# Kernel optimization log

Measured on AMD Instinct MI355X. Metric: run time of the kernel, lower is better.

## Reference

```python
import jax, jax.numpy as jnp
import numpy as np

# Performer/FAVOR+ style linear attention constants (from module __init__)
A_CONST = 0.1
S_CONST = 1.0
B_CONST = (S_CONST * (1.0 - 4.0 * A_CONST)) ** 0.5  # sqrt(0.6)
C_CONST = -(S_CONST + 1.0) / 2.0                    # -1.0

R = 256     # number of random features
D = 64      # head / feature dim
L = 65536   # sequence length
DV = 64     # value dim
SCALE = 0.125  # keep ||q||^2 ~ 1 so exp stays well-conditioned


def setup_inputs() -> dict:
    key = jax.random.key(0)
    kq, kk, kv, kw = jax.random.split(key, 4)
    Q = jax.random.normal(kq, (D, L), dtype=jnp.float32) * SCALE
    K = jax.random.normal(kk, (D, L), dtype=jnp.float32) * SCALE
    V = jax.random.normal(kv, (L, DV), dtype=jnp.float32)
    W = jax.random.normal(kw, (R, D), dtype=jnp.float32)  # random feature projections
    return {"Q": Q, "K": K, "V": V, "W": W}


def _phi(W, X, c):
    # X: [d, L]; W: [r, d] -> features [r, L]
    d = X.shape[0]
    D_norm = (1.0 - 4.0 * A_CONST) ** (d / 4.0)  # pow(pow(1-4A,0.25), d)
    sq = jnp.sum(X * X, axis=0)                  # [L], diag of X^T X
    return D_norm * jnp.exp(A_CONST + B_CONST * (W @ X) + c * sq)


def reference(Q, K, V, W):
    phiK = _phi(W, K, C_CONST * S_CONST)  # f2: [r, Lk]
    kv = phiK @ V                          # [r, dv]
    phiQ = _phi(W, Q, C_CONST)             # f1: [r, Lq]
    return phiQ.T @ kv                     # [Lq, dv]
```

## Files before the change

### kernel.cpp

```cpp
#include <hip/hip_runtime.h>

typedef _Float16 f16;
typedef __attribute__((ext_vector_type(8))) _Float16 f16x8;
typedef __attribute__((ext_vector_type(4))) _Float16 f16x4;
typedef __attribute__((ext_vector_type(4))) float f32x4;

#define BARRIER()                                              \
    do {                                                       \
        asm volatile("s_waitcnt lgkmcnt(0)" ::: "memory");     \
        __builtin_amdgcn_s_barrier();                          \
        __builtin_amdgcn_sched_barrier(0);                     \
    } while (0)

namespace {
constexpr int kL   = 65536;
constexpr int kR   = 256;
constexpr int kD   = 64;
constexpr int kDV  = 64;

constexpr int kABlocks = 512;
constexpr int kBBlocks = 512;
constexpr int kRBlocks = 128;

constexpr float kBc   = 0.7745966692414834f;
constexpr float kBase0 = -1.1417405264f;
constexpr float kOutScale = 9.5367431640625e-7f;
}

__global__ __launch_bounds__(512, 2)
void favor_kv(const float* __restrict__ Kg, const float* __restrict__ Vg,
              const float* __restrict__ Wg, f16* __restrict__ partials)
{
    __shared__ f16 sXt[2][64 * 64];
    __shared__ f16 sVt[2][64 * 64];
    __shared__ f16 sPhi[256 * 64];
    __shared__ float sRed[2][8 * 64];
    __shared__ float sRedT[2][64];

    const int tid  = threadIdx.x;
    const int w    = tid >> 6;
    const int lane = tid & 63;
    const int l15  = lane & 15;
    const int lhi  = lane >> 4;
    const int blk  = blockIdx.x;
    const int lblk = blk * 128;

    const int scol  = lane;
    const int dbase = w * 8;
    const int wr = w >> 1;
    const int wc = w & 1;

    float ka[2][8], va[2][8];
#pragma unroll
    for (int c = 0; c < 2; ++c) {
        const int l0 = lblk + c * 64;
#pragma unroll
        for (int j = 0; j < 8; ++j) ka[c][j] = Kg[(dbase + j) * kL + l0 + scol];
#pragma unroll
        for (int j = 0; j < 8; ++j) va[c][j] = Vg[(size_t)(l0 + dbase + j) * kDV + scol];
    }

    f16x8 wfrag[2][2];
#pragma unroll
    for (int ri = 0; ri < 2; ++ri)
#pragma unroll
        for (int ks = 0; ks < 2; ++ks) {
            const float* p = Wg + (32 * w + 16 * ri + l15) * kD + 32 * ks + 8 * lhi;
            f16x8 v;
#pragma unroll
            for (int j = 0; j < 8; ++j) v[j] = (f16)p[j];
            wfrag[ri][ks] = v;
        }

    f32x4 acc[4][2];
#pragma unroll
    for (int a = 0; a < 4; ++a)
#pragma unroll
        for (int d = 0; d < 2; ++d) { f32x4 z0 = {0.f, 0.f, 0.f, 0.f}; acc[a][d] = z0; }

    auto stage = [&](int c) {
        float s = 0.f;
        f16x8 hk, hv;
#pragma unroll
        for (int j = 0; j < 8; ++j) {
            const float x = ka[c][j];
            s += x * x;
            hk[j] = (f16)x;
            hv[j] = (f16)va[c][j];
        }
        sRed[c][w * 64 + scol] = s;
        *(f16x8*)&sXt[c][scol * 64 + (dbase ^ ((scol & 7) << 3))] = hk;
        *(f16x8*)&sVt[c][scol * 64 + (dbase ^ ((scol & 7) << 3))] = hv;
    };

    auto norms = [&](int c) {
        float sqv = 0.f;
#pragma unroll
        for (int g = 0; g < 8; ++g) sqv += sRed[c][g * 64 + lane];
        sRedT[c][lane] = sqv;
    };

    auto zphi = [&](int c) {
        f16x8 bfr[2][4];
#pragma unroll
        for (int ks = 0; ks < 2; ++ks)
#pragma unroll
            for (int lf = 0; lf < 4; ++lf) {
                const int row = 16 * lf + l15;
                bfr[ks][lf] = *(const f16x8*)&sXt[c][row * 64 + ((32 * ks + 8 * lhi) ^ ((row & 7) << 3))];
            }
#pragma unroll
        for (int ri = 0; ri < 2; ++ri) {
            f32x4 z[4];
#pragma unroll
            for (int lf = 0; lf < 4; ++lf) { f32x4 z0 = {0.f, 0.f, 0.f, 0.f}; z[lf] = z0; }
            __builtin_amdgcn_s_setprio(1);
#pragma unroll
            for (int ks = 0; ks < 2; ++ks)
#pragma unroll
                for (int lf = 0; lf < 4; ++lf)
                    z[lf] = __builtin_amdgcn_mfma_f32_16x16x32_f16(bfr[ks][lf], wfrag[ri][ks], z[lf], 0, 0, 0);
            __builtin_amdgcn_s_setprio(0);
            const int r = 32 * w + 16 * ri + l15;
#pragma unroll
            for (int lf = 0; lf < 4; ++lf) {
                const f32x4 sq4 = *(const f32x4*)&sRedT[c][16 * lf + 4 * lhi];
                f16x4 ph;
#pragma unroll
                for (int j = 0; j < 4; ++j)
                    ph[j] = (f16)__expf(fmaf(z[lf][j], kBc, kBase0 - sq4[j]));
                const int lbase = 16 * lf + 4 * lhi;
                *(f16x4*)&sPhi[r * 64 + (lbase ^ ((r & 7) << 3))] = ph;
            }
        }
    };

    auto pv = [&](int c) {
        __builtin_amdgcn_s_setprio(1);
#pragma unroll
        for (int ks = 0; ks < 2; ++ks) {
            f16x8 af[4], bf[2];
#pragma unroll
            for (int ai = 0; ai < 4; ++ai) {
                const int r = 64 * wr + 16 * ai + l15;
                af[ai] = *(const f16x8*)&sPhi[r * 64 + ((32 * ks + 8 * lhi) ^ ((r & 7) << 3))];
            }
#pragma unroll
            for (int di = 0; di < 2; ++di) {
                const int dv = 32 * wc + 16 * di + l15;
                bf[di] = *(const f16x8*)&sVt[c][dv * 64 + ((32 * ks + 8 * lhi) ^ ((dv & 7) << 3))];
            }
#pragma unroll
            for (int ai = 0; ai < 4; ++ai)
#pragma unroll
                for (int di = 0; di < 2; ++di)
                    acc[ai][di] = __builtin_amdgcn_mfma_f32_16x16x32_f16(af[ai], bf[di], acc[ai][di], 0, 0, 0);
        }
        __builtin_amdgcn_s_setprio(0);
    };

    stage(0);
    BARRIER();
    norms(0);
    zphi(0);
    stage(1);
    BARRIER();
    norms(1);
    pv(0);
    BARRIER();
    zphi(1);
    BARRIER();
    pv(1);

    f16* po = partials + (size_t)blk * (kR * kDV);
#pragma unroll
    for (int ai = 0; ai < 4; ++ai)
#pragma unroll
        for (int di = 0; di < 2; ++di) {
            const int dv = 32 * wc + 16 * di + l15;
            f16x4 pk;
#pragma unroll
            for (int j = 0; j < 4; ++j) pk[j] = (f16)acc[ai][di][j];
            *(f16x4*)&po[dv * kR + 64 * wr + 16 * ai + 4 * lhi] = pk;
        }
}

__global__ __launch_bounds__(512)
void favor_reduce(const f16* __restrict__ partials, f16* __restrict__ kvT,
                  const float* __restrict__ Wg, f16* __restrict__ Wp)
{
    __shared__ float sAcc[32][128];
    const int tid  = threadIdx.x;
    const int slot = tid & 15;
    const int g    = tid >> 4;

    if (blockIdx.x == 0) {
#pragma unroll
        for (int it = 0; it < 4; ++it) {
            const int idx    = tid + it * 512;
            const int fragid = idx >> 6;
            const int ln     = idx & 63;
            const int rf = fragid >> 1, ks = fragid & 1;
            const float* src = Wg + (16 * rf + (ln & 15)) * kD + 32 * ks + 8 * (ln >> 4);
            f16x8 v;
#pragma unroll
            for (int j = 0; j < 8; ++j) v[j] = (f16)src[j];
            *(f16x8*)&Wp[(size_t)idx * 8] = v;
        }
    }

    const size_t obase = (size_t)blockIdx.x * 128 + slot * 8;
    float a[8] = {0.f, 0.f, 0.f, 0.f, 0.f, 0.f, 0.f, 0.f};
#pragma unroll 4
    for (int i = 0; i < 16; ++i) {
        const int s = g * 16 + i;
        const f16x8 v = *(const f16x8*)&partials[(size_t)s * (kR * kDV) + obase];
#pragma unroll
        for (int j = 0; j < 8; ++j) a[j] += (float)v[j];
    }
#pragma unroll
    for (int j = 0; j < 8; ++j) sAcc[g][slot * 8 + j] = a[j];
    __syncthreads();

    if (tid < 128) {
        float tot = 0.f;
#pragma unroll
        for (int gg = 0; gg < 32; ++gg) tot += sAcc[gg][tid];
        kvT[(size_t)blockIdx.x * 128 + tid] = (f16)tot;
    }
}

__global__ __launch_bounds__(512, 2)
void favor_out(const float* __restrict__ Qg, const f16* __restrict__ Wp,
               const f16* __restrict__ kvT, float* __restrict__ outg)
{
    __shared__ f16 sXt[2][64 * 64];
    __shared__ f16 sPhiT[64 * 256];
    __shared__ float sRed[2][8 * 64];

    const int tid  = threadIdx.x;
    const int w    = tid >> 6;
    const int lane = tid & 63;
    const int l15  = lane & 15;
    const int lhi  = lane >> 4;
    const int blk  = blockIdx.x;
    const int lblk = blk * 128;

    const int scol  = lane;
    const int dbase = w * 8;
    const int lfo = w >> 1;
    const int dvh = w & 1;

    float qa[2][8];
#pragma unroll
    for (int c = 0; c < 2; ++c)
#pragma unroll
        for (int j = 0; j < 8; ++j)
            qa[c][j] = Qg[(dbase + j) * kL + lblk + c * 64 + scol];

    f16x8 kvf[2][8];
#pragma unroll
    for (int di = 0; di < 2; ++di) {
        const int dv = 32 * dvh + 16 * di + l15;
#pragma unroll
        for (int ks = 0; ks < 8; ++ks)
            kvf[di][ks] = *(const f16x8*)&kvT[dv * kR + 32 * ks + 8 * lhi];
    }

    f16x8 wfrag[2][2];
#pragma unroll
    for (int ri = 0; ri < 2; ++ri)
#pragma unroll
        for (int ks = 0; ks < 2; ++ks)
            wfrag[ri][ks] = *(const f16x8*)&Wp[(size_t)((((2 * w + ri) * 2 + ks) * 64) + lane) * 8];

    auto stageQ = [&](int c) {
        float s = 0.f;
        f16x8 hq;
#pragma unroll
        for (int j = 0; j < 8; ++j) {
            const float x = qa[c][j];
            s += x * x;
            hq[j] = (f16)x;
        }
        sRed[c][w * 64 + scol] = s;
        *(f16x8*)&sXt[c][scol * 64 + (dbase ^ ((scol & 7) << 3))] = hq;
    };

    auto zphiQ = [&](int c) {
        float sqv = 0.f;
#pragma unroll
        for (int g = 0; g < 8; ++g) sqv += sRed[c][g * 64 + lane];
        float tbase[4];
#pragma unroll
        for (int lf = 0; lf < 4; ++lf)
            tbase[lf] = kBase0 - __shfl(sqv, lf * 16 + l15, 64);

        f16x8 bfr[2][4];
#pragma unroll
        for (int ks = 0; ks < 2; ++ks)
#pragma unroll
            for (int lf = 0; lf < 4; ++lf) {
                const int row = 16 * lf + l15;
                bfr[ks][lf] = *(const f16x8*)&sXt[c][row * 64 + ((32 * ks + 8 * lhi) ^ ((row & 7) << 3))];
            }
#pragma unroll
        for (int ri = 0; ri < 2; ++ri) {
            f32x4 z[4];
#pragma unroll
            for (int lf = 0; lf < 4; ++lf) { f32x4 z0 = {0.f, 0.f, 0.f, 0.f}; z[lf] = z0; }
            __builtin_amdgcn_s_setprio(1);
#pragma unroll
            for (int ks = 0; ks < 2; ++ks)
#pragma unroll
                for (int lf = 0; lf < 4; ++lf)
                    z[lf] = __builtin_amdgcn_mfma_f32_16x16x32_f16(wfrag[ri][ks], bfr[ks][lf], z[lf], 0, 0, 0);
            __builtin_amdgcn_s_setprio(0);
            const int r0 = 32 * w + 16 * ri + 4 * lhi;
#pragma unroll
            for (int lf = 0; lf < 4; ++lf) {
                const int lc = 16 * lf + l15;
                f16x4 ph;
#pragma unroll
                for (int j = 0; j < 4; ++j)
                    ph[j] = (f16)__expf(fmaf(z[lf][j], kBc, tbase[lf]));
                *(f16x4*)&sPhiT[lc * 256 + (r0 ^ ((lc & 7) << 3))] = ph;
            }
        }
    };

    auto pvOut = [&](int c) {
        f32x4 oA[2], oB[2];
        { f32x4 z0 = {0.f, 0.f, 0.f, 0.f}; oA[0] = z0; oA[1] = z0; oB[0] = z0; oB[1] = z0; }
        const int lrow = 16 * lfo + l15;
        __builtin_amdgcn_s_setprio(1);
#pragma unroll
        for (int ks = 0; ks < 4; ++ks) {
            const f16x8 afA = *(const f16x8*)&sPhiT[lrow * 256 + ((32 * ks + 8 * lhi) ^ ((lrow & 7) << 3))];
            const f16x8 afB = *(const f16x8*)&sPhiT[lrow * 256 + ((32 * (ks + 4) + 8 * lhi) ^ ((lrow & 7) << 3))];
#pragma unroll
            for (int di = 0; di < 2; ++di) {
                oA[di] = __builtin_amdgcn_mfma_f32_16x16x32_f16(afA, kvf[di][ks], oA[di], 0, 0, 0);
                oB[di] = __builtin_amdgcn_mfma_f32_16x16x32_f16(afB, kvf[di][ks + 4], oB[di], 0, 0, 0);
            }
        }
        __builtin_amdgcn_s_setprio(0);
        const int l0 = lblk + c * 64;
#pragma unroll
        for (int di = 0; di < 2; ++di) {
            const f32x4 o2 = oA[di] + oB[di];
#pragma unroll
            for (int j = 0; j < 4; ++j) {
                const int ll = 16 * lfo + 4 * lhi + j;
                const int dv = 32 * dvh + 16 * di + l15;
                outg[(size_t)(l0 + ll) * kDV + dv] = o2[j] * kOutScale;
            }
        }
    };

    stageQ(0);
    BARRIER();
    zphiQ(0);
    stageQ(1);
    BARRIER();
    pvOut(0);
    BARRIER();
    zphiQ(1);
    BARRIER();
    pvOut(1);
}

extern "C" void kernel_launch(void* const* d_in, const int* in_sizes, int n_in,
                              void* d_out, int out_size, void* d_ws, size_t ws_size,
                              hipStream_t stream)
{
    const float* Q = (const float*)d_in[0];
    const float* K = (const float*)d_in[1];
    const float* V = (const float*)d_in[2];
    const float* W = (const float*)d_in[3];
    float* out = (float*)d_out;

    f16* partials = (f16*)d_ws;
    f16* kvT = (f16*)((char*)d_ws + (size_t)kABlocks * kR * kDV * sizeof(f16));
    f16* Wp  = kvT + (size_t)kR * kDV;

    favor_kv<<<kABlocks, 512, 0, stream>>>(K, V, W, partials);
    favor_reduce<<<kRBlocks, 512, 0, stream>>>(partials, kvT, W, Wp);
    favor_out<<<kBBlocks, 512, 0, stream>>>(Q, Wp, kvT, out);

    (void)in_sizes; (void)n_in; (void)out_size; (void)ws_size;
}
```

Baseline: 42.70 us.

## Process four L-chunks per block with double-buffered register prefetch

Each block of both the K/V and Q kernels now walks four 64-column chunks of the sequence instead of two. Global loads for chunk c+2 are issued while chunk c is being computed, with shared-memory and register buffers ping-ponged by chunk parity. This halves the block count, which halves the partials the reduce kernel must sum and amortizes the W/kv fragment setup over more work. The cost is fewer blocks to fill the GPU (256 blocks) and extra barriers per chunk.

New measurement: 36.20 us. 15.2% less time.

```diff
diff --git a/kernel.cpp b/kernel.cpp
--- a/kernel.cpp
+++ b/kernel.cpp
@@ -18,8 +18,9 @@
 constexpr int kD   = 64;
 constexpr int kDV  = 64;
 
-constexpr int kABlocks = 512;
-constexpr int kBBlocks = 512;
+constexpr int kChunks  = 4;
+constexpr int kABlocks = 256;
+constexpr int kBBlocks = 256;
 constexpr int kRBlocks = 128;
 
 constexpr float kBc   = 0.7745966692414834f;
@@ -43,7 +44,7 @@
     const int l15  = lane & 15;
     const int lhi  = lane >> 4;
     const int blk  = blockIdx.x;
-    const int lblk = blk * 128;
+    const int lblk = blk * (64 * kChunks);
 
     const int scol  = lane;
     const int dbase = w * 8;
@@ -51,14 +52,17 @@
     const int wc = w & 1;
 
     float ka[2][8], va[2][8];
-#pragma unroll
-    for (int c = 0; c < 2; ++c) {
+    auto issueLoads = [&](int c) {
         const int l0 = lblk + c * 64;
-#pragma unroll
-        for (int j = 0; j < 8; ++j) ka[c][j] = Kg[(dbase + j) * kL + l0 + scol];
-#pragma unroll
-        for (int j = 0; j < 8; ++j) va[c][j] = Vg[(size_t)(l0 + dbase + j) * kDV + scol];
-    }
+        const int p  = c & 1;
+#pragma unroll
+        for (int j = 0; j < 8; ++j) ka[p][j] = Kg[(dbase + j) * kL + l0 + scol];
+#pragma unroll
+        for (int j = 0; j < 8; ++j) va[p][j] = Vg[(size_t)(l0 + dbase + j) * kDV + scol];
+    };
+
+    issueLoads(0);
+    issueLoads(1);
 
     f16x8 wfrag[2][2];
 #pragma unroll
@@ -79,35 +83,38 @@
         for (int d = 0; d < 2; ++d) { f32x4 z0 = {0.f, 0.f, 0.f, 0.f}; acc[a][d] = z0; }
 
     auto stage = [&](int c) {
+        const int p = c & 1;
         float s = 0.f;
         f16x8 hk, hv;
 #pragma unroll
         for (int j = 0; j < 8; ++j) {
-            const float x = ka[c][j];
+            const float x = ka[p][j];
             s += x * x;
             hk[j] = (f16)x;
-            hv[j] = (f16)va[c][j];
-        }
-        sRed[c][w * 64 + scol] = s;
-        *(f16x8*)&sXt[c][scol * 64 + (dbase ^ ((scol & 7) << 3))] = hk;
-        *(f16x8*)&sVt[c][scol * 64 + (dbase ^ ((scol & 7) << 3))] = hv;
+            hv[j] = (f16)va[p][j];
+        }
+        sRed[p][w * 64 + scol] = s;
+        *(f16x8*)&sXt[p][scol * 64 + (dbase ^ ((scol & 7) << 3))] = hk;
+        *(f16x8*)&sVt[p][scol * 64 + (dbase ^ ((scol & 7) << 3))] = hv;
     };
 
     auto norms = [&](int c) {
+        const int p = c & 1;
         float sqv = 0.f;
 #pragma unroll
-        for (int g = 0; g < 8; ++g) sqv += sRed[c][g * 64 + lane];
-        sRedT[c][lane] = sqv;
+        for (int g = 0; g < 8; ++g) sqv += sRed[p][g * 64 + lane];
+        sRedT[p][lane] = sqv;
     };
 
     auto zphi = [&](int c) {
+        const int p = c & 1;
         f16x8 bfr[2][4];
 #pragma unroll
         for (int ks = 0; ks < 2; ++ks)
 #pragma unroll
             for (int lf = 0; lf < 4; ++lf) {
                 const int row = 16 * lf + l15;
-                bfr[ks][lf] = *(const f16x8*)&sXt[c][row * 64 + ((32 * ks + 8 * lhi) ^ ((row & 7) << 3))];
+                bfr[ks][lf] = *(const f16x8*)&sXt[p][row * 64 + ((32 * ks + 8 * lhi) ^ ((row & 7) << 3))];
             }
 #pragma unroll
         for (int ri = 0; ri < 2; ++ri) {
@@ -124,7 +131,7 @@
             const int r = 32 * w + 16 * ri + l15;
 #pragma unroll
             for (int lf = 0; lf < 4; ++lf) {
-                const f32x4 sq4 = *(const f32x4*)&sRedT[c][16 * lf + 4 * lhi];
+                const f32x4 sq4 = *(const f32x4*)&sRedT[p][16 * lf + 4 * lhi];
                 f16x4 ph;
 #pragma unroll
                 for (int j = 0; j < 4; ++j)
@@ -136,6 +143,7 @@
     };
 
     auto pv = [&](int c) {
+        const int p = c & 1;
         __builtin_amdgcn_s_setprio(1);
 #pragma unroll
         for (int ks = 0; ks < 2; ++ks) {
@@ -148,7 +156,7 @@
 #pragma unroll
             for (int di = 0; di < 2; ++di) {
                 const int dv = 32 * wc + 16 * di + l15;
-                bf[di] = *(const f16x8*)&sVt[c][dv * 64 + ((32 * ks + 8 * lhi) ^ ((dv & 7) << 3))];
+                bf[di] = *(const f16x8*)&sVt[p][dv * 64 + ((32 * ks + 8 * lhi) ^ ((dv & 7) << 3))];
             }
 #pragma unroll
             for (int ai = 0; ai < 4; ++ai)
@@ -161,16 +169,16 @@
 
     stage(0);
     BARRIER();
-    norms(0);
-    zphi(0);
-    stage(1);
-    BARRIER();
-    norms(1);
-    pv(0);
-    BARRIER();
-    zphi(1);
-    BARRIER();
-    pv(1);
+#pragma unroll
+    for (int c = 0; c < kChunks; ++c) {
+        norms(c);
+        zphi(c);
+        if (c + 1 < kChunks) stage(c + 1);
+        if (c + 2 < kChunks) issueLoads(c + 2);
+        BARRIER();
+        pv(c);
+        BARRIER();
+    }
 
     f16* po = partials + (size_t)blk * (kR * kDV);
 #pragma unroll
@@ -212,8 +220,8 @@
     const size_t obase = (size_t)blockIdx.x * 128 + slot * 8;
     float a[8] = {0.f, 0.f, 0.f, 0.f, 0.f, 0.f, 0.f, 0.f};
 #pragma unroll 4
-    for (int i = 0; i < 16; ++i) {
-        const int s = g * 16 + i;
+    for (int i = 0; i < 8; ++i) {
+        const int s = g * 8 + i;
         const f16x8 v = *(const f16x8*)&partials[(size_t)s * (kR * kDV) + obase];
 #pragma unroll
         for (int j = 0; j < 8; ++j) a[j] += (float)v[j];
@@ -244,7 +252,7 @@
     const int l15  = lane & 15;
     const int lhi  = lane >> 4;
     const int blk  = blockIdx.x;
-    const int lblk = blk * 128;
+    const int lblk = blk * (64 * kChunks);
 
     const int scol  = lane;
     const int dbase = w * 8;
@@ -252,11 +260,15 @@
     const int dvh = w & 1;
 
     float qa[2][8];
-#pragma unroll
-    for (int c = 0; c < 2; ++c)
-#pragma unroll
-        for (int j = 0; j < 8; ++j)
-            qa[c][j] = Qg[(dbase + j) * kL + lblk + c * 64 + scol];
+    auto issueLoads = [&](int c) {
+        const int l0 = lblk + c * 64;
+        const int p  = c & 1;
+#pragma unroll
+        for (int j = 0; j < 8; ++j) qa[p][j] = Qg[(dbase + j) * kL + l0 + scol];
+    };
+
+    issueLoads(0);
+    issueLoads(1);
 
     f16x8 kvf[2][8];
 #pragma unroll
@@ -275,22 +287,24 @@
             wfrag[ri][ks] = *(const f16x8*)&Wp[(size_t)((((2 * w + ri) * 2 + ks) * 64) + lane) * 8];
 
     auto stageQ = [&](int c) {
+        const int p = c & 1;
         float s = 0.f;
         f16x8 hq;
 #pragma unroll
         for (int j = 0; j < 8; ++j) {
-            const float x = qa[c][j];
+            const float x = qa[p][j];
             s += x * x;
             hq[j] = (f16)x;
         }
-        sRed[c][w * 64 + scol] = s;
-        *(f16x8*)&sXt[c][scol * 64 + (dbase ^ ((scol & 7) << 3))] = hq;
+        sRed[p][w * 64 + scol] = s;
+        *(f16x8*)&sXt[p][scol * 64 + (dbase ^ ((scol & 7) << 3))] = hq;
     };
 
     auto zphiQ = [&](int c) {
+        const int p = c & 1;
         float sqv = 0.f;
 #pragma unroll
-        for (int g = 0; g < 8; ++g) sqv += sRed[c][g * 64 + lane];
+        for (int g = 0; g < 8; ++g) sqv += sRed[p][g * 64 + lane];
         float tbase[4];
 #pragma unroll
         for (int lf = 0; lf < 4; ++lf)
@@ -302,7 +316,7 @@
 #pragma unroll
             for (int lf = 0; lf < 4; ++lf) {
                 const int row = 16 * lf + l15;
-                bfr[ks][lf] = *(const f16x8*)&sXt[c][row * 64 + ((32 * ks + 8 * lhi) ^ ((row & 7) << 3))];
+                bfr[ks][lf] = *(const f16x8*)&sXt[p][row * 64 + ((32 * ks + 8 * lhi) ^ ((row & 7) << 3))];
             }
 #pragma unroll
         for (int ri = 0; ri < 2; ++ri) {
@@ -360,14 +374,15 @@
 
     stageQ(0);
     BARRIER();
-    zphiQ(0);
-    stageQ(1);
-    BARRIER();
-    pvOut(0);
-    BARRIER();
-    zphiQ(1);
-    BARRIER();
-    pvOut(1);
+#pragma unroll
+    for (int c = 0; c < kChunks; ++c) {
+        zphiQ(c);
+        if (c + 1 < kChunks) stageQ(c + 1);
+        if (c + 2 < kChunks) issueLoads(c + 2);
+        BARRIER();
+        pvOut(c);
+        BARRIER();
+    }
 }
 
 extern "C" void kernel_launch(void* const* d_in, const int* in_sizes, int n_in,
```
